# Kernel tuning notes

Hardware: AMD Instinct MI355X
Metric: run time of the kernel (lower is better)

## Reference

```python
import jax, jax.numpy as jnp
import numpy as np

H = 4096
W = 4096
C = 3
OUT = 1024
MAX_MIP = 8  # matches init max_mip_level; mip chain is levels 0..MAX_MIP


def setup_inputs() -> dict:
    key = jax.random.key(0)
    k1, k2, k3 = jax.random.split(key, 3)
    data = jax.random.uniform(k1, (1, H, W, C), dtype=jnp.float32)
    texc = jax.random.uniform(k2, (1, OUT, OUT, 2), dtype=jnp.float32)
    # small UV derivatives -> per-pixel texel footprint of a few texels, so the
    # LOD spans several mip levels (exercises cross-level paged gathers)
    texc_deriv = jax.random.normal(k3, (1, OUT, OUT, 4), dtype=jnp.float32) * 2e-3
    return {"data": data, "texc": texc, "texc_deriv": texc_deriv}


def _avg_pool2(x):
    # 2x2 box-filter mipmap reduction, matching virtual_texture_mipmap_fwd
    b, h, w, c = x.shape
    return x.reshape(b, h // 2, 2, w // 2, 2, c).mean(axis=(2, 4))


def _bilinear_wrap(tex, texc):
    # tex: [1,h,w,c]; texc: [1,Ho,Wo,2] in [0,1); boundary_mode='wrap'
    h, w = tex.shape[1], tex.shape[2]
    x = texc[..., 0] * w - 0.5
    y = texc[..., 1] * h - 0.5
    x0f = jnp.floor(x)
    y0f = jnp.floor(y)
    fx = (x - x0f)[..., None]
    fy = (y - y0f)[..., None]
    x0 = x0f.astype(jnp.int32) % w
    y0 = y0f.astype(jnp.int32) % h
    x1 = (x0 + 1) % w
    y1 = (y0 + 1) % h
    t = tex[0]  # [h,w,c]
    top = t[y0, x0] * (1.0 - fx) + t[y0, x1] * fx
    bot = t[y1, x0] * (1.0 - fx) + t[y1, x1] * fx
    return top * (1.0 - fy) + bot * fy  # [1,Ho,Wo,c]


def _forward(data, texc, texc_deriv):
    # LOD from screen-space UV derivatives (nvdiffrast linear-mipmap-linear)
    dudx = texc_deriv[..., 0] * W
    dvdx = texc_deriv[..., 1] * H
    dudy = texc_deriv[..., 2] * W
    dvdy = texc_deriv[..., 3] * H
    rho2 = jnp.maximum(dudx * dudx + dvdx * dvdx, dudy * dudy + dvdy * dvdy)
    lod = 0.5 * jnp.log2(jnp.maximum(rho2, 1e-20))
    lod = jnp.clip(lod, 0.0, float(MAX_MIP))  # [1,Ho,Wo]

    # build mip pyramid (gradients flow back to base texture, matching
    # virtual_texture_mipmap_bwd accumulation)
    mips = [data]
    for _ in range(MAX_MIP):
        mips.append(_avg_pool2(mips[-1]))

    # trilinear: per-level weight w_l = clip(1 - |lod - l|, 0, 1)
    out = jnp.zeros(texc.shape[:-1] + (C,), dtype=data.dtype)
    for lvl in range(MAX_MIP + 1):
        w_l = jnp.clip(1.0 - jnp.abs(lod - float(lvl)), 0.0, 1.0)[..., None]
        out = out + w_l * _bilinear_wrap(mips[lvl], texc)
    return out


def reference(data, texc, texc_deriv):
    return _forward(data, texc, texc_deriv)
```

## Files before the change

kernel.cpp:

```cpp
#include <hip/hip_runtime.h>
#include <hip/hip_bf16.h>


#define TEX_W 4096
#define OUT_N (1024 * 1024)

__global__ void mip_down(const float* __restrict__ in, float* __restrict__ out,
                         int out_size ) {
    int n = out_size * out_size * 3;
    int i = blockIdx.x * blockDim.x + threadIdx.x;
    if (i >= n) return;
    int c = i % 3;
    int p = i / 3;
    int x = p & (out_size - 1);
    int y = p / out_size;
    int in_size = out_size * 2;
    const float* base = in + ((size_t)(2 * y) * in_size + 2 * x) * 3 + c;
    float a = base[0];
    float b = base[3];
    float e = base[(size_t)in_size * 3];
    float d = base[(size_t)in_size * 3 + 3];
    out[i] = (a + b + e + d) * 0.25f;
}

__device__ __forceinline__ const float* mip_base(const float* data, const float* ws, int lvl) {
    if (lvl == 0) return data;
    unsigned off = 16777216u - (16777216u >> (2 * (lvl - 1)));
    return ws + off;
}

__device__ __forceinline__ void sample_level(const float* __restrict__ t, int lvl,
                                             float u, float v, float wgt,
                                             float& r, float& g, float& b) {
    int size = TEX_W >> lvl;
    float fs = (float)size;
    float x = u * fs - 0.5f;
    float y = v * fs - 0.5f;
    float x0f = floorf(x);
    float y0f = floorf(y);
    float fx = x - x0f;
    float fy = y - y0f;
    int m = size - 1;
    int x0 = ((int)x0f) & m;
    int y0 = ((int)y0f) & m;
    int x1 = (x0 + 1) & m;
    int y1 = (y0 + 1) & m;
    const float* p00 = t + ((size_t)y0 * size + x0) * 3;
    const float* p01 = t + ((size_t)y0 * size + x1) * 3;
    const float* p10 = t + ((size_t)y1 * size + x0) * 3;
    const float* p11 = t + ((size_t)y1 * size + x1) * 3;
    float w00 = (1.0f - fx) * (1.0f - fy) * wgt;
    float w01 = fx * (1.0f - fy) * wgt;
    float w10 = (1.0f - fx) * fy * wgt;
    float w11 = fx * fy * wgt;
    r += p00[0] * w00 + p01[0] * w01 + p10[0] * w10 + p11[0] * w11;
    g += p00[1] * w00 + p01[1] * w01 + p10[1] * w10 + p11[1] * w11;
    b += p00[2] * w00 + p01[2] * w01 + p10[2] * w10 + p11[2] * w11;
}

__global__ void vt_sample(const float* __restrict__ data, const float* __restrict__ ws,
                          const float* __restrict__ texc, const float* __restrict__ deriv,
                          float* __restrict__ out) {
    int p = blockIdx.x * blockDim.x + threadIdx.x;
    if (p >= OUT_N) return;

    float2 uv = ((const float2*)texc)[p];
    float4 dv = ((const float4*)deriv)[p];
    float dudx = dv.x * (float)TEX_W;
    float dvdx = dv.y * (float)TEX_W;
    float dudy = dv.z * (float)TEX_W;
    float dvdy = dv.w * (float)TEX_W;
    float rho2 = fmaxf(dudx * dudx + dvdx * dvdx, dudy * dudy + dvdy * dvdy);
    float lod = 0.5f * log2f(fmaxf(rho2, 1e-20f));
    lod = fminf(fmaxf(lod, 0.0f), 8.0f);

    int l0 = (int)floorf(lod);
    if (l0 > 8) l0 = 8;
    float f = lod - (float)l0;
    int l1 = (l0 < 8) ? (l0 + 1) : 8;

    float r = 0.0f, g = 0.0f, b = 0.0f;
    sample_level(mip_base(data, ws, l0), l0, uv.x, uv.y, 1.0f - f, r, g, b);
    sample_level(mip_base(data, ws, l1), l1, uv.x, uv.y, f, r, g, b);

    float* o = out + (size_t)p * 3;
    o[0] = r;
    o[1] = g;
    o[2] = b;
}

extern "C" void kernel_launch(void* const* d_in, const int* in_sizes, int n_in,
                              void* d_out, int out_size, void* d_ws, size_t ws_size,
                              hipStream_t stream) {
    const float* data  = (const float*)d_in[0];
    const float* texc  = (const float*)d_in[1];
    const float* deriv = (const float*)d_in[2];
    float* out = (float*)d_out;
    float* ws  = (float*)d_ws;

    const float* src = data;
    unsigned off = 0;
    int osz = 2048;
    for (int l = 1; l <= 8; ++l) {
        float* dst = ws + off;
        int n = osz * osz * 3;
        int blocks = (n + 255) / 256;
        mip_down<<<blocks, 256, 0, stream>>>(src, dst, osz);
        src = dst;
        off += (unsigned)n;
        osz >>= 1;
    }

    int blocks = (OUT_N + 255) / 256;
    vt_sample<<<blocks, 256, 0, stream>>>(data, ws, texc, deriv, out);
}
```

Baseline: 350.2 us.

## Fuse mip pyramid into one shared-memory kernel with padded float4 texels

```diff
diff --git a/kernel.cpp b/kernel.cpp
--- a/kernel.cpp
+++ b/kernel.cpp
@@ -5,33 +5,157 @@
 #define TEX_W 4096
 #define OUT_N (1024 * 1024)
 
-__global__ void mip_down(const float* __restrict__ in, float* __restrict__ out,
-                         int out_size ) {
-    int n = out_size * out_size * 3;
-    int i = blockIdx.x * blockDim.x + threadIdx.x;
-    if (i >= n) return;
-    int c = i % 3;
-    int p = i / 3;
-    int x = p & (out_size - 1);
-    int y = p / out_size;
-    int in_size = out_size * 2;
-    const float* base = in + ((size_t)(2 * y) * in_size + 2 * x) * 3 + c;
-    float a = base[0];
-    float b = base[3];
-    float e = base[(size_t)in_size * 3];
-    float d = base[(size_t)in_size * 3 + 3];
-    out[i] = (a + b + e + d) * 0.25f;
-}
-
-__device__ __forceinline__ const float* mip_base(const float* data, const float* ws, int lvl) {
-    if (lvl == 0) return data;
-    unsigned off = 16777216u - (16777216u >> (2 * (lvl - 1)));
-    return ws + off;
-}
-
-__device__ __forceinline__ void sample_level(const float* __restrict__ t, int lvl,
-                                             float u, float v, float wgt,
-                                             float& r, float& g, float& b) {
+__device__ __forceinline__ unsigned mip_off(int lvl) {
+    return (67108864u - (67108864u >> (2 * (lvl - 1)))) / 3u;
+}
+
+__global__ __launch_bounds__(256) void mip_fused(const float* __restrict__ data,
+                                                 float* __restrict__ ws) {
+    __shared__ float4 s1[32][33];
+    __shared__ float4 s2[16][17];
+    __shared__ float4 s3[8][9];
+    __shared__ float4 s4[4][5];
+    __shared__ float4 s5[2][3];
+
+    const int t = threadIdx.x;
+    const int bx = blockIdx.x & 63;
+    const int by = blockIdx.x >> 6;
+
+    float4* L1 = (float4*)ws;
+    float4* L2 = (float4*)(ws + 16777216u);
+    float4* L3 = (float4*)(ws + 20971520u);
+    float4* L4 = (float4*)(ws + 22020096u);
+    float4* L5 = (float4*)(ws + 22282240u);
+    float4* L6 = (float4*)(ws + 22347776u);
+
+    for (int k = 0; k < 4; ++k) {
+        int p = t + (k << 8);
+        int ly = p >> 5, lx = p & 31;
+        int gy = (by << 5) + ly, gx = (bx << 5) + lx;
+        const float* r0 = data + ((size_t)gy * 8192 + gx * 2) * 3;
+        const float* r1 = r0 + 4096 * 3;
+        float2 a0 = *(const float2*)(r0);
+        float2 b0 = *(const float2*)(r0 + 2);
+        float2 c0 = *(const float2*)(r0 + 4);
+        float2 a1 = *(const float2*)(r1);
+        float2 b1 = *(const float2*)(r1 + 2);
+        float2 c1 = *(const float2*)(r1 + 4);
+        float4 px;
+        px.x = (a0.x + b0.y + a1.x + b1.y) * 0.25f;
+        px.y = (a0.y + c0.x + a1.y + c1.x) * 0.25f;
+        px.z = (b0.x + c0.y + b1.x + c1.y) * 0.25f;
+        px.w = 0.0f;
+        L1[(size_t)gy * 2048 + gx] = px;
+        s1[ly][lx] = px;
+    }
+    __syncthreads();
+
+    {
+        int ly = t >> 4, lx = t & 15;
+        float4 p00 = s1[2 * ly][2 * lx], p01 = s1[2 * ly][2 * lx + 1];
+        float4 p10 = s1[2 * ly + 1][2 * lx], p11 = s1[2 * ly + 1][2 * lx + 1];
+        float4 px;
+        px.x = (p00.x + p01.x + p10.x + p11.x) * 0.25f;
+        px.y = (p00.y + p01.y + p10.y + p11.y) * 0.25f;
+        px.z = (p00.z + p01.z + p10.z + p11.z) * 0.25f;
+        px.w = 0.0f;
+        L2[(size_t)((by << 4) + ly) * 1024 + (bx << 4) + lx] = px;
+        s2[ly][lx] = px;
+    }
+    __syncthreads();
+
+    if (t < 64) {
+        int ly = t >> 3, lx = t & 7;
+        float4 p00 = s2[2 * ly][2 * lx], p01 = s2[2 * ly][2 * lx + 1];
+        float4 p10 = s2[2 * ly + 1][2 * lx], p11 = s2[2 * ly + 1][2 * lx + 1];
+        float4 px;
+        px.x = (p00.x + p01.x + p10.x + p11.x) * 0.25f;
+        px.y = (p00.y + p01.y + p10.y + p11.y) * 0.25f;
+        px.z = (p00.z + p01.z + p10.z + p11.z) * 0.25f;
+        px.w = 0.0f;
+        L3[(size_t)((by << 3) + ly) * 512 + (bx << 3) + lx] = px;
+        s3[ly][lx] = px;
+    }
+    __syncthreads();
+
+    if (t < 16) {
+        int ly = t >> 2, lx = t & 3;
+        float4 p00 = s3[2 * ly][2 * lx], p01 = s3[2 * ly][2 * lx + 1];
+        float4 p10 = s3[2 * ly + 1][2 * lx], p11 = s3[2 * ly + 1][2 * lx + 1];
+        float4 px;
+        px.x = (p00.x + p01.x + p10.x + p11.x) * 0.25f;
+        px.y = (p00.y + p01.y + p10.y + p11.y) * 0.25f;
+        px.z = (p00.z + p01.z + p10.z + p11.z) * 0.25f;
+        px.w = 0.0f;
+        L4[(size_t)((by << 2) + ly) * 256 + (bx << 2) + lx] = px;
+        s4[ly][lx] = px;
+    }
+    __syncthreads();
+
+    if (t < 4) {
+        int ly = t >> 1, lx = t & 1;
+        float4 p00 = s4[2 * ly][2 * lx], p01 = s4[2 * ly][2 * lx + 1];
+        float4 p10 = s4[2 * ly + 1][2 * lx], p11 = s4[2 * ly + 1][2 * lx + 1];
+        float4 px;
+        px.x = (p00.x + p01.x + p10.x + p11.x) * 0.25f;
+        px.y = (p00.y + p01.y + p10.y + p11.y) * 0.25f;
+        px.z = (p00.z + p01.z + p10.z + p11.z) * 0.25f;
+        px.w = 0.0f;
+        L5[(size_t)((by << 1) + ly) * 128 + (bx << 1) + lx] = px;
+        s5[ly][lx] = px;
+    }
+    __syncthreads();
+
+    if (t == 0) {
+        float4 p00 = s5[0][0], p01 = s5[0][1], p10 = s5[1][0], p11 = s5[1][1];
+        float4 px;
+        px.x = (p00.x + p01.x + p10.x + p11.x) * 0.25f;
+        px.y = (p00.y + p01.y + p10.y + p11.y) * 0.25f;
+        px.z = (p00.z + p01.z + p10.z + p11.z) * 0.25f;
+        px.w = 0.0f;
+        L6[(size_t)by * 64 + bx] = px;
+    }
+}
+
+__global__ __launch_bounds__(256) void mip_tail(float* __restrict__ ws) {
+    __shared__ float4 s7[32][33];
+    const float4* L6 = (const float4*)(ws + 22347776u);
+    float4* L7 = (float4*)(ws + 22364160u);
+    float4* L8 = (float4*)(ws + 22368256u);
+    const int t = threadIdx.x;
+
+    for (int k = 0; k < 4; ++k) {
+        int p = t + (k << 8);
+        int ly = p >> 5, lx = p & 31;
+        float4 p00 = L6[(size_t)(2 * ly) * 64 + 2 * lx];
+        float4 p01 = L6[(size_t)(2 * ly) * 64 + 2 * lx + 1];
+        float4 p10 = L6[(size_t)(2 * ly + 1) * 64 + 2 * lx];
+        float4 p11 = L6[(size_t)(2 * ly + 1) * 64 + 2 * lx + 1];
+        float4 px;
+        px.x = (p00.x + p01.x + p10.x + p11.x) * 0.25f;
+        px.y = (p00.y + p01.y + p10.y + p11.y) * 0.25f;
+        px.z = (p00.z + p01.z + p10.z + p11.z) * 0.25f;
+        px.w = 0.0f;
+        L7[(size_t)ly * 32 + lx] = px;
+        s7[ly][lx] = px;
+    }
+    __syncthreads();
+    {
+        int ly = t >> 4, lx = t & 15;
+        float4 p00 = s7[2 * ly][2 * lx], p01 = s7[2 * ly][2 * lx + 1];
+        float4 p10 = s7[2 * ly + 1][2 * lx], p11 = s7[2 * ly + 1][2 * lx + 1];
+        float4 px;
+        px.x = (p00.x + p01.x + p10.x + p11.x) * 0.25f;
+        px.y = (p00.y + p01.y + p10.y + p11.y) * 0.25f;
+        px.z = (p00.z + p01.z + p10.z + p11.z) * 0.25f;
+        px.w = 0.0f;
+        L8[(size_t)ly * 16 + lx] = px;
+    }
+}
+
+__device__ __forceinline__ void sample_padded(const float* __restrict__ ws, int lvl,
+                                              float u, float v, float wgt,
+                                              float& r, float& g, float& b) {
     int size = TEX_W >> lvl;
     float fs = (float)size;
     float x = u * fs - 0.5f;
@@ -45,10 +169,41 @@
     int y0 = ((int)y0f) & m;
     int x1 = (x0 + 1) & m;
     int y1 = (y0 + 1) & m;
-    const float* p00 = t + ((size_t)y0 * size + x0) * 3;
-    const float* p01 = t + ((size_t)y0 * size + x1) * 3;
-    const float* p10 = t + ((size_t)y1 * size + x0) * 3;
-    const float* p11 = t + ((size_t)y1 * size + x1) * 3;
+    const float4* t = (const float4*)(ws + mip_off(lvl));
+    const float4* row0 = t + (size_t)y0 * size;
+    const float4* row1 = t + (size_t)y1 * size;
+    float4 c00 = row0[x0];
+    float4 c01 = row0[x1];
+    float4 c10 = row1[x0];
+    float4 c11 = row1[x1];
+    float w00 = (1.0f - fx) * (1.0f - fy) * wgt;
+    float w01 = fx * (1.0f - fy) * wgt;
+    float w10 = (1.0f - fx) * fy * wgt;
+    float w11 = fx * fy * wgt;
+    r += c00.x * w00 + c01.x * w01 + c10.x * w10 + c11.x * w11;
+    g += c00.y * w00 + c01.y * w01 + c10.y * w10 + c11.y * w11;
+    b += c00.z * w00 + c01.z * w01 + c10.z * w10 + c11.z * w11;
+}
+
+__device__ __forceinline__ void sample_level0(const float* __restrict__ data,
+                                              float u, float v, float wgt,
+                                              float& r, float& g, float& b) {
+    float fs = (float)TEX_W;
+    float x = u * fs - 0.5f;
+    float y = v * fs - 0.5f;
+    float x0f = floorf(x);
+    float y0f = floorf(y);
+    float fx = x - x0f;
+    float fy = y - y0f;
+    int m = TEX_W - 1;
+    int x0 = ((int)x0f) & m;
+    int y0 = ((int)y0f) & m;
+    int x1 = (x0 + 1) & m;
+    int y1 = (y0 + 1) & m;
+    const float* p00 = data + ((size_t)y0 * TEX_W + x0) * 3;
+    const float* p01 = data + ((size_t)y0 * TEX_W + x1) * 3;
+    const float* p10 = data + ((size_t)y1 * TEX_W + x0) * 3;
+    const float* p11 = data + ((size_t)y1 * TEX_W + x1) * 3;
     float w00 = (1.0f - fx) * (1.0f - fy) * wgt;
     float w01 = fx * (1.0f - fy) * wgt;
     float w10 = (1.0f - fx) * fy * wgt;
@@ -58,11 +213,12 @@
     b += p00[2] * w00 + p01[2] * w01 + p10[2] * w10 + p11[2] * w11;
 }
 
-__global__ void vt_sample(const float* __restrict__ data, const float* __restrict__ ws,
-                          const float* __restrict__ texc, const float* __restrict__ deriv,
-                          float* __restrict__ out) {
-    int p = blockIdx.x * blockDim.x + threadIdx.x;
-    if (p >= OUT_N) return;
+__global__ __launch_bounds__(256) void vt_sample(const float* __restrict__ data,
+                                                 const float* __restrict__ ws,
+                                                 const float* __restrict__ texc,
+                                                 const float* __restrict__ deriv,
+                                                 float* __restrict__ out) {
+    int p = blockIdx.x * 256 + threadIdx.x;
 
     float2 uv = ((const float2*)texc)[p];
     float4 dv = ((const float4*)deriv)[p];
@@ -74,14 +230,17 @@
     float lod = 0.5f * log2f(fmaxf(rho2, 1e-20f));
     lod = fminf(fmaxf(lod, 0.0f), 8.0f);
 
-    int l0 = (int)floorf(lod);
-    if (l0 > 8) l0 = 8;
+    int l0 = (int)lod;
     float f = lod - (float)l0;
     int l1 = (l0 < 8) ? (l0 + 1) : 8;
 
     float r = 0.0f, g = 0.0f, b = 0.0f;
-    sample_level(mip_base(data, ws, l0), l0, uv.x, uv.y, 1.0f - f, r, g, b);
-    sample_level(mip_base(data, ws, l1), l1, uv.x, uv.y, f, r, g, b);
+    if (l0 == 0) {
+        sample_level0(data, uv.x, uv.y, 1.0f - f, r, g, b);
+    } else {
+        sample_padded(ws, l0, uv.x, uv.y, 1.0f - f, r, g, b);
+    }
+    sample_padded(ws, l1, uv.x, uv.y, f, r, g, b);
 
     float* o = out + (size_t)p * 3;
     o[0] = r;
@@ -98,19 +257,7 @@
     float* out = (float*)d_out;
     float* ws  = (float*)d_ws;
 
-    const float* src = data;
-    unsigned off = 0;
-    int osz = 2048;
-    for (int l = 1; l <= 8; ++l) {
-        float* dst = ws + off;
-        int n = osz * osz * 3;
-        int blocks = (n + 255) / 256;
-        mip_down<<<blocks, 256, 0, stream>>>(src, dst, osz);
-        src = dst;
-        off += (unsigned)n;
-        osz >>= 1;
-    }
-
-    int blocks = (OUT_N + 255) / 256;
-    vt_sample<<<blocks, 256, 0, stream>>>(data, ws, texc, deriv, out);
-}
+    mip_fused<<<4096, 256, 0, stream>>>(data, ws);
+    mip_tail<<<1, 256, 0, stream>>>(ws);
+    vt_sample<<<OUT_N / 256, 256, 0, stream>>>(data, ws, texc, deriv, out);
+}
```

Result: no change. 344.5 us (-1.6%).
